# Kernel optimization log

Measured on AMD Instinct MI355X. Metric: run time of the kernel, lower is better.

The kernel has to match this reference:

```python
import jax, jax.numpy as jnp
import numpy as np

B, N, F_IN, T, K, F_OUT = 16, 1536, 64, 12, 3, 64


def setup_inputs() -> dict:
    key = jax.random.key(0)
    k1, k2, k3, k4 = jax.random.split(key, 4)
    x = jax.random.normal(k1, (B, N, F_IN, T), dtype=jnp.float32)
    spatial_attention = jax.random.uniform(k2, (B, N, N), dtype=jnp.float32)
    # stacked Chebyshev polynomials T_0..T_{K-1}, each (N, N); scaled like
    # normalized-Laplacian polynomials to keep magnitudes sane
    cheb = jax.random.normal(k3, (K, N, N), dtype=jnp.float32) * (1.0 / np.sqrt(N))
    # Theta initialized with torch.rand -> uniform[0,1)
    Theta = jax.random.uniform(k4, (K, F_IN, F_OUT), dtype=jnp.float32)
    return {"x": x, "spatial_attention": spatial_attention, "cheb": cheb, "Theta": Theta}


def reference(x, spatial_attention, cheb, Theta):
    # x: (B, N, F_in, T); spatial_attention: (B, N, N)
    # cheb: (K, N, N); Theta: (K, F_in, F_out)
    # Original per (t, k): ((T_k * At)^T @ x[..., t]) @ Theta_k, summed over k, relu.
    # Vectorized over all timesteps at once; small fixed K loop avoids a
    # (K, B, N, N) intermediate.
    n_cheb = cheb.shape[0]
    acc = jnp.zeros(x.shape[:2] + (Theta.shape[-1], x.shape[-1]), dtype=x.dtype)  # (B,N,F_out,T)
    for k in range(n_cheb):
        t_k_with_at = cheb[k][None, :, :] * spatial_attention          # (B, N, N)
        # transpose over node dims is folded into the einsum: sum over source node n
        rhs = jnp.einsum("bnm,bnft->bmft", t_k_with_at, x)             # (B, N, F_in, T)
        acc = acc + jnp.einsum("bmft,fo->bmot", rhs, Theta[k])         # (B, N, F_out, T)
    return jax.nn.relu(acc)
```

## Files before the change

kernel.cpp:

```cpp
#include <hip/hip_runtime.h>
#include <hip/hip_bf16.h>
#include <stdint.h>


#define B_    16
#define N_    1536
#define FIN_  64
#define T_    12
#define K_    3
#define FOUT_ 64
#define C_    768

typedef float          f32x4 __attribute__((ext_vector_type(4)));
typedef short          s16x8 __attribute__((ext_vector_type(8)));
typedef unsigned short u16x4 __attribute__((ext_vector_type(4)));

__device__ __forceinline__ unsigned short f2bf(float f) {
    unsigned int u = __builtin_bit_cast(unsigned int, f);
    return (unsigned short)((u + 0x8000u) >> 16);
}

__global__ __launch_bounds__(256) void s1_theta(const float* __restrict__ x,
                                                const float* __restrict__ Theta,
                                                unsigned short* __restrict__ Y) {
    __shared__ __align__(16) float xt[16][772];

    int bid = blockIdx.x;
    int nc = bid % 96, b = bid / 96;
    int n0 = nc * 16;
    int tid = threadIdx.x;

    const float* xg = x + (size_t)(b * N_ + n0) * 768;
#pragma unroll
    for (int i = 0; i < 12; ++i) {
        int c = i * 256 + tid;
        int row = c / 192, col = (c % 192) * 4;
        f32x4 v = *(const f32x4*)(xg + (size_t)c * 4);
        *(f32x4*)&xt[row][col] = v;
    }
    __syncthreads();

    int oo = tid >> 4, nn = tid & 15;
    const float* th = Theta + oo * 4;

    float acc[3][4][12];
#pragma unroll
    for (int k = 0; k < 3; ++k)
#pragma unroll
        for (int j = 0; j < 4; ++j)
#pragma unroll
            for (int t = 0; t < 12; ++t) acc[k][j][t] = 0.f;

    for (int f = 0; f < 64; ++f) {
        f32x4 xv0 = *(const f32x4*)&xt[nn][f * 12];
        f32x4 xv1 = *(const f32x4*)&xt[nn][f * 12 + 4];
        f32x4 xv2 = *(const f32x4*)&xt[nn][f * 12 + 8];
#pragma unroll
        for (int k = 0; k < 3; ++k) {
            f32x4 tv = *(const f32x4*)(th + (size_t)(k * 64 + f) * 64);
#pragma unroll
            for (int j = 0; j < 4; ++j) {
#pragma unroll
                for (int t = 0; t < 4; ++t) {
                    acc[k][j][t]     += tv[j] * xv0[t];
                    acc[k][j][t + 4] += tv[j] * xv1[t];
                    acc[k][j][t + 8] += tv[j] * xv2[t];
                }
            }
        }
    }

    unsigned short* yp = Y + (size_t)b * (K_ * C_ * (size_t)N_) + n0 + nn;
#pragma unroll
    for (int k = 0; k < 3; ++k)
#pragma unroll
        for (int j = 0; j < 4; ++j)
#pragma unroll
            for (int t = 0; t < 12; ++t) {
                int c = (oo * 4 + j) * 12 + t;
                yp[((size_t)k * C_ + c) * N_] = f2bf(acc[k][j][t]);
            }
}

#define NN_ ((size_t)N_ * N_)
#define CN_ ((size_t)C_ * N_)

__global__ __launch_bounds__(256, 2) void s2_gemm(const float* __restrict__ At,
                                                  const float* __restrict__ cheb,
                                                  const unsigned short* __restrict__ Y,
                                                  float* __restrict__ out) {
    __shared__ __align__(16) unsigned short Alds[2][128 * 40];
    __shared__ __align__(16) unsigned short Blds[2][128 * 32];

    int hb = blockIdx.x;
    int lb = (hb & 7) * 144 + (hb >> 3);
    int mt = lb % 12;
    int ct = (lb / 12) % 6;
    int b  = lb / 72;
    int m0 = mt * 128, c0 = ct * 128;

    int tid  = threadIdx.x;
    int lane = tid & 63, wave = tid >> 6;
    int wr = (wave >> 1) * 64, wc = (wave & 1) * 64;
    int l15 = lane & 15;

    int q = tid & 7, g = tid >> 3;

    const float* cb = cheb + (size_t)(q * 4) * N_ + (m0 + g * 4);
    const float* ab = At + (size_t)b * NN_ + (size_t)(q * 4) * N_ + (m0 + g * 4);
    const unsigned short* yb = Y + (size_t)(b * K_) * CN_
                                 + (size_t)(c0 + (tid >> 2)) * N_ + (tid & 3) * 8;

    int awb = g * 320 + q * 8;
    int bwb = (tid >> 2) * 64 + (((tid & 3) ^ ((tid >> 2) & 3)) << 4);
    int ard = (wr + l15) * 80 + (lane >> 4) * 16;
    int brd = (wc + l15) * 64 + (((lane >> 4) ^ (lane & 3)) << 4);

    f32x4 acc[4][4];
#pragma unroll
    for (int mi = 0; mi < 4; ++mi)
#pragma unroll
        for (int ci = 0; ci < 4; ++ci) acc[mi][ci] = (f32x4)0.f;

    f32x4 cvA[4], avA[4]; s16x8 yA0, yA1;
    f32x4 cvB[4], avB[4]; s16x8 yB0, yB1;

#define PF(CV, AV, Y0v, Y1v, DNT, KC) do {                                   \
    const float* cbk_ = cb + (size_t)(KC) * NN_ + (size_t)(DNT) * 32 * N_;   \
    const float* abk_ = ab + (size_t)(DNT) * 32 * N_;                        \
    const unsigned short* ybk_ = yb + (size_t)(KC) * CN_ + (DNT) * 32;       \
    _Pragma("unroll") for (int j = 0; j < 4; ++j) {                          \
        CV[j] = *(const f32x4*)(cbk_ + (size_t)j * N_);                      \
        AV[j] = *(const f32x4*)(abk_ + (size_t)j * N_); }                    \
    Y0v = *(const s16x8*)(ybk_);                                             \
    Y1v = *(const s16x8*)(ybk_ + (size_t)64 * N_); } while (0)

#define STEP(CV, AV, Y0v, Y1v, PCV, PAV, PY0, PY1, P, PDNT, PKC, DOPF) do {  \
    char* Ab_ = (char*)Alds[P];                                              \
    char* Bb_ = (char*)Blds[P];                                              \
    f32x4 w_[4];                                                             \
    _Pragma("unroll") for (int j = 0; j < 4; ++j) w_[j] = CV[j] * AV[j];     \
    _Pragma("unroll") for (int i = 0; i < 4; ++i) {                          \
        u16x4 pk_ = { f2bf(w_[0][i]), f2bf(w_[1][i]),                        \
                      f2bf(w_[2][i]), f2bf(w_[3][i]) };                      \
        *(u16x4*)(Ab_ + awb + i * 80) = pk_; }                               \
    *(s16x8*)(Bb_ + bwb)        = Y0v;                                       \
    *(s16x8*)(Bb_ + bwb + 4096) = Y1v;                                       \
    if (DOPF) { PF(PCV, PAV, PY0, PY1, PDNT, PKC); }                         \
    asm volatile("s_waitcnt lgkmcnt(0)" ::: "memory");                       \
    __builtin_amdgcn_s_barrier();                                            \
    __builtin_amdgcn_sched_barrier(0);                                       \
    s16x8 af_[4], bv_[4];                                                    \
    _Pragma("unroll") for (int mi = 0; mi < 4; ++mi)                         \
        af_[mi] = *(const s16x8*)((const char*)Ab_ + ard + mi * 1280);       \
    _Pragma("unroll") for (int ci = 0; ci < 4; ++ci)                         \
        bv_[ci] = *(const s16x8*)((const char*)Bb_ + brd + ci * 1024);       \
    _Pragma("unroll") for (int mi = 0; mi < 4; ++mi)                         \
        _Pragma("unroll") for (int ci = 0; ci < 4; ++ci)                     \
            acc[mi][ci] = __builtin_amdgcn_mfma_f32_16x16x32_bf16(           \
                af_[mi], bv_[ci], acc[mi][ci], 0, 0, 0);                     \
    } while (0)

    PF(cvA, avA, yA0, yA1, 0, 0);

    for (int it2 = 0; it2 < 24; ++it2) {
        bool more = (it2 != 23);
        STEP(cvA, avA, yA0, yA1, cvB, avB, yB0, yB1, 0, 0, 1, true);
        STEP(cvB, avB, yB0, yB1, cvA, avA, yA0, yA1, 1, 0, 2, true);
        STEP(cvA, avA, yA0, yA1, cvB, avB, yB0, yB1, 0, 1, 0, true);
        STEP(cvB, avB, yB0, yB1, cvA, avA, yA0, yA1, 1, 1, 1, true);
        STEP(cvA, avA, yA0, yA1, cvB, avB, yB0, yB1, 0, 1, 2, true);
        STEP(cvB, avB, yB0, yB1, cvA, avA, yA0, yA1, 1, 2, 0, more);
        cb += (size_t)64 * N_;
        ab += (size_t)64 * N_;
        yb += 64;
    }
#undef PF
#undef STEP

    int rbase = (lane >> 4) * 4;
#pragma unroll
    for (int mi = 0; mi < 4; ++mi) {
#pragma unroll
        for (int ci = 0; ci < 4; ++ci) {
            int m = m0 + wr + mi * 16 + rbase;
            int c = c0 + wc + ci * 16 + l15;
            float* op = out + (size_t)(b * N_ + m) * C_ + c;
#pragma unroll
            for (int r = 0; r < 4; ++r) {
                float v = acc[mi][ci][r];
                op[(size_t)r * C_] = v > 0.f ? v : 0.f;
            }
        }
    }
}

extern "C" void kernel_launch(void* const* d_in, const int* in_sizes, int n_in,
                              void* d_out, int out_size, void* d_ws, size_t ws_size,
                              hipStream_t stream) {
    const float* x    = (const float*)d_in[0];
    const float* At   = (const float*)d_in[1];
    const float* cheb = (const float*)d_in[2];
    const float* Th   = (const float*)d_in[3];
    unsigned short* Y = (unsigned short*)d_ws;
    float* out = (float*)d_out;

    s1_theta<<<dim3(B_ * 96),     dim3(256), 0, stream>>>(x, Th, Y);
    s2_gemm <<<dim3(B_ * 12 * 6), dim3(256), 0, stream>>>(At, cheb, Y, out);
}
```

Measured before the change: 1.037 ms.

## Stage Y tiles via direct global-to-LDS loads and restructure GEMM pipeline

The B operand (bf16 Y) is now moved straight from global memory into LDS with global_load_lds instead of passing through registers, and the A weight tile for the next step is built into the alternate LDS buffer before the current MFMA block. Prefetched register copies drop from two sets to one, which frees registers, and launch bounds rise to 3 blocks per SM to raise occupancy. s1_theta now loops over k with a smaller accumulator to reduce register pressure. The risks are spills under the tighter register budget and ordering hazards between the async LDS loads and the barriers.

Result: faster. 1.003 ms (-3.3%).

```diff
diff --git a/kernel.cpp b/kernel.cpp
--- a/kernel.cpp
+++ b/kernel.cpp
@@ -10,6 +10,8 @@
 #define K_    3
 #define FOUT_ 64
 #define C_    768
+#define NN_ ((size_t)N_ * N_)
+#define CN_ ((size_t)C_ * N_)
 
 typedef float          f32x4 __attribute__((ext_vector_type(4)));
 typedef short          s16x8 __attribute__((ext_vector_type(8)));
@@ -18,6 +20,12 @@
 __device__ __forceinline__ unsigned short f2bf(float f) {
     unsigned int u = __builtin_bit_cast(unsigned int, f);
     return (unsigned short)((u + 0x8000u) >> 16);
+}
+
+__device__ __forceinline__ void gload_lds16(const void* g, void* l) {
+    __builtin_amdgcn_global_load_lds(
+        (const __attribute__((address_space(1))) unsigned*)g,
+        (__attribute__((address_space(3))) unsigned*)l, 16, 0, 0);
 }
 
 __global__ __launch_bounds__(256) void s1_theta(const float* __restrict__ x,
@@ -35,57 +43,47 @@
     for (int i = 0; i < 12; ++i) {
         int c = i * 256 + tid;
         int row = c / 192, col = (c % 192) * 4;
-        f32x4 v = *(const f32x4*)(xg + (size_t)c * 4);
-        *(f32x4*)&xt[row][col] = v;
+        *(f32x4*)&xt[row][col] = *(const f32x4*)(xg + (size_t)c * 4);
     }
     __syncthreads();
 
     int oo = tid >> 4, nn = tid & 15;
-    const float* th = Theta + oo * 4;
-
-    float acc[3][4][12];
-#pragma unroll
-    for (int k = 0; k < 3; ++k)
+    unsigned short* yp = Y + (size_t)b * (K_ * CN_) + n0 + nn;
+
+    for (int k = 0; k < 3; ++k) {
+        const float* th = Theta + (size_t)k * 4096 + oo * 4;
+        float acc[4][12];
 #pragma unroll
         for (int j = 0; j < 4; ++j)
 #pragma unroll
-            for (int t = 0; t < 12; ++t) acc[k][j][t] = 0.f;
-
-    for (int f = 0; f < 64; ++f) {
-        f32x4 xv0 = *(const f32x4*)&xt[nn][f * 12];
-        f32x4 xv1 = *(const f32x4*)&xt[nn][f * 12 + 4];
-        f32x4 xv2 = *(const f32x4*)&xt[nn][f * 12 + 8];
-#pragma unroll
-        for (int k = 0; k < 3; ++k) {
-            f32x4 tv = *(const f32x4*)(th + (size_t)(k * 64 + f) * 64);
+            for (int t = 0; t < 12; ++t) acc[j][t] = 0.f;
+
+        for (int f = 0; f < 64; ++f) {
+            f32x4 xv0 = *(const f32x4*)&xt[nn][f * 12];
+            f32x4 xv1 = *(const f32x4*)&xt[nn][f * 12 + 4];
+            f32x4 xv2 = *(const f32x4*)&xt[nn][f * 12 + 8];
+            f32x4 tv  = *(const f32x4*)(th + (size_t)f * 64);
 #pragma unroll
             for (int j = 0; j < 4; ++j) {
 #pragma unroll
                 for (int t = 0; t < 4; ++t) {
-                    acc[k][j][t]     += tv[j] * xv0[t];
-                    acc[k][j][t + 4] += tv[j] * xv1[t];
-                    acc[k][j][t + 8] += tv[j] * xv2[t];
+                    acc[j][t]     += tv[j] * xv0[t];
+                    acc[j][t + 4] += tv[j] * xv1[t];
+                    acc[j][t + 8] += tv[j] * xv2[t];
                 }
             }
         }
-    }
-
-    unsigned short* yp = Y + (size_t)b * (K_ * C_ * (size_t)N_) + n0 + nn;
-#pragma unroll
-    for (int k = 0; k < 3; ++k)
 #pragma unroll
         for (int j = 0; j < 4; ++j)
 #pragma unroll
             for (int t = 0; t < 12; ++t) {
                 int c = (oo * 4 + j) * 12 + t;
-                yp[((size_t)k * C_ + c) * N_] = f2bf(acc[k][j][t]);
+                yp[((size_t)k * C_ + c) * N_] = f2bf(acc[j][t]);
             }
-}
-
-#define NN_ ((size_t)N_ * N_)
-#define CN_ ((size_t)C_ * N_)
-
-__global__ __launch_bounds__(256, 2) void s2_gemm(const float* __restrict__ At,
+    }
+}
+
+__global__ __launch_bounds__(256, 3) void s2_gemm(const float* __restrict__ At,
                                                   const float* __restrict__ cheb,
                                                   const unsigned short* __restrict__ Y,
                                                   float* __restrict__ out) {
@@ -108,11 +106,13 @@
 
     const float* cb = cheb + (size_t)(q * 4) * N_ + (m0 + g * 4);
     const float* ab = At + (size_t)b * NN_ + (size_t)(q * 4) * N_ + (m0 + g * 4);
+
+    int lrow = lane >> 2;
+    int lchunk = (lane & 3) ^ (lrow & 3);
     const unsigned short* yb = Y + (size_t)(b * K_) * CN_
-                                 + (size_t)(c0 + (tid >> 2)) * N_ + (tid & 3) * 8;
+                               + (size_t)(c0 + wave * 16 + lrow) * N_ + lchunk * 8;
 
     int awb = g * 320 + q * 8;
-    int bwb = (tid >> 2) * 64 + (((tid & 3) ^ ((tid >> 2) & 3)) << 4);
     int ard = (wr + l15) * 80 + (lane >> 4) * 16;
     int brd = (wc + l15) * 64 + (((lane >> 4) ^ (lane & 3)) << 4);
 
@@ -122,60 +122,66 @@
 #pragma unroll
         for (int ci = 0; ci < 4; ++ci) acc[mi][ci] = (f32x4)0.f;
 
-    f32x4 cvA[4], avA[4]; s16x8 yA0, yA1;
-    f32x4 cvB[4], avB[4]; s16x8 yB0, yB1;
-
-#define PF(CV, AV, Y0v, Y1v, DNT, KC) do {                                   \
+    f32x4 cv[4], av[4];
+
+#define PFREG(DNT, KC) do {                                                  \
     const float* cbk_ = cb + (size_t)(KC) * NN_ + (size_t)(DNT) * 32 * N_;   \
     const float* abk_ = ab + (size_t)(DNT) * 32 * N_;                        \
-    const unsigned short* ybk_ = yb + (size_t)(KC) * CN_ + (DNT) * 32;       \
     _Pragma("unroll") for (int j = 0; j < 4; ++j) {                          \
-        CV[j] = *(const f32x4*)(cbk_ + (size_t)j * N_);                      \
-        AV[j] = *(const f32x4*)(abk_ + (size_t)j * N_); }                    \
-    Y0v = *(const s16x8*)(ybk_);                                             \
-    Y1v = *(const s16x8*)(ybk_ + (size_t)64 * N_); } while (0)
-
-#define STEP(CV, AV, Y0v, Y1v, PCV, PAV, PY0, PY1, P, PDNT, PKC, DOPF) do {  \
-    char* Ab_ = (char*)Alds[P];                                              \
-    char* Bb_ = (char*)Blds[P];                                              \
+        cv[j] = *(const f32x4*)(cbk_ + (size_t)j * N_);                      \
+        av[j] = *(const f32x4*)(abk_ + (size_t)j * N_); } } while (0)
+
+#define YDMA(PN, DNT, KC) do {                                               \
+    const unsigned short* ys_ = yb + (size_t)(KC) * CN_ + (DNT) * 32;        \
+    char* bl_ = (char*)Blds[PN] + wave * 1024;                               \
+    gload_lds16(ys_, bl_);                                                   \
+    gload_lds16(ys_ + (size_t)64 * N_, bl_ + 4096); } while (0)
+
+#define WBUILD(PN) do {                                                      \
     f32x4 w_[4];                                                             \
-    _Pragma("unroll") for (int j = 0; j < 4; ++j) w_[j] = CV[j] * AV[j];     \
+    _Pragma("unroll") for (int j = 0; j < 4; ++j) w_[j] = cv[j] * av[j];     \
     _Pragma("unroll") for (int i = 0; i < 4; ++i) {                          \
         u16x4 pk_ = { f2bf(w_[0][i]), f2bf(w_[1][i]),                        \
                       f2bf(w_[2][i]), f2bf(w_[3][i]) };                      \
-        *(u16x4*)(Ab_ + awb + i * 80) = pk_; }                               \
-    *(s16x8*)(Bb_ + bwb)        = Y0v;                                       \
-    *(s16x8*)(Bb_ + bwb + 4096) = Y1v;                                       \
-    if (DOPF) { PF(PCV, PAV, PY0, PY1, PDNT, PKC); }                         \
-    asm volatile("s_waitcnt lgkmcnt(0)" ::: "memory");                       \
-    __builtin_amdgcn_s_barrier();                                            \
-    __builtin_amdgcn_sched_barrier(0);                                       \
+        *(u16x4*)((char*)Alds[PN] + awb + i * 80) = pk_; } } while (0)
+
+#define STEP(P, DNTn, KCn, DNTnn, KCnn, DOSTAGE, DOLOAD) do {                \
+    if (DOSTAGE) { YDMA((P) ^ 1, DNTn, KCn); WBUILD((P) ^ 1); }              \
+    if (DOLOAD)  { PFREG(DNTnn, KCnn); }                                     \
+    const char* Ab_ = (const char*)Alds[P];                                  \
+    const char* Bb_ = (const char*)Blds[P];                                  \
     s16x8 af_[4], bv_[4];                                                    \
     _Pragma("unroll") for (int mi = 0; mi < 4; ++mi)                         \
-        af_[mi] = *(const s16x8*)((const char*)Ab_ + ard + mi * 1280);       \
+        af_[mi] = *(const s16x8*)(Ab_ + ard + mi * 1280);                    \
     _Pragma("unroll") for (int ci = 0; ci < 4; ++ci)                         \
-        bv_[ci] = *(const s16x8*)((const char*)Bb_ + brd + ci * 1024);       \
+        bv_[ci] = *(const s16x8*)(Bb_ + brd + ci * 1024);                    \
     _Pragma("unroll") for (int mi = 0; mi < 4; ++mi)                         \
         _Pragma("unroll") for (int ci = 0; ci < 4; ++ci)                     \
             acc[mi][ci] = __builtin_amdgcn_mfma_f32_16x16x32_bf16(           \
                 af_[mi], bv_[ci], acc[mi][ci], 0, 0, 0);                     \
-    } while (0)
-
-    PF(cvA, avA, yA0, yA1, 0, 0);
+    __syncthreads(); } while (0)
+
+    PFREG(0, 0);
+    YDMA(0, 0, 0);
+    WBUILD(0);
+    PFREG(0, 1);
+    __syncthreads();
 
     for (int it2 = 0; it2 < 24; ++it2) {
         bool more = (it2 != 23);
-        STEP(cvA, avA, yA0, yA1, cvB, avB, yB0, yB1, 0, 0, 1, true);
-        STEP(cvB, avB, yB0, yB1, cvA, avA, yA0, yA1, 1, 0, 2, true);
-        STEP(cvA, avA, yA0, yA1, cvB, avB, yB0, yB1, 0, 1, 0, true);
-        STEP(cvB, avB, yB0, yB1, cvA, avA, yA0, yA1, 1, 1, 1, true);
-        STEP(cvA, avA, yA0, yA1, cvB, avB, yB0, yB1, 0, 1, 2, true);
-        STEP(cvB, avB, yB0, yB1, cvA, avA, yA0, yA1, 1, 2, 0, more);
+        STEP(0, 0, 1, 0, 2, true, true);
+        STEP(1, 0, 2, 1, 0, true, true);
+        STEP(0, 1, 0, 1, 1, true, true);
+        STEP(1, 1, 1, 1, 2, true, true);
+        STEP(0, 1, 2, 2, 0, true, more);
+        STEP(1, 2, 0, 2, 1, more, more);
         cb += (size_t)64 * N_;
         ab += (size_t)64 * N_;
         yb += 64;
     }
-#undef PF
+#undef PFREG
+#undef YDMA
+#undef WBUILD
 #undef STEP
 
     int rbase = (lane >> 4) * 4;
```
